# Kernel tuning notes

Hardware: AMD Instinct MI355X
Metric: run time of the kernel (lower is better)

## Reference

```python
import jax, jax.numpy as jnp
import numpy as np
import math
from jax import lax

B, C, L = 8, 512, 1024
NCONV, K, H = 4, 7, 8
DH = C // H
EPS = 1e-5
NEG = -1e30


def layer_norm(x, g, b):
    mu = jnp.mean(x, axis=-1, keepdims=True)
    var = jnp.mean(jnp.square(x - mu), axis=-1, keepdims=True)
    return (x - mu) * lax.rsqrt(var + EPS) * g + b


def positional_encoding(d, n):
    pos = jnp.arange(n, dtype=jnp.float32)[:, None]                     # [n,1]
    div = jnp.exp(jnp.arange(0, d, 2, dtype=jnp.float32) * (-math.log(10000.0) / d))
    ang = pos * div                                                      # [n,d/2]
    pe = jnp.zeros((d, n), dtype=jnp.float32)
    pe = pe.at[0::2].set(jnp.sin(ang).T).at[1::2].set(jnp.cos(ang).T)
    return pe                                                            # [d,n]


def setup_inputs() -> dict:
    key = jax.random.key(0)
    ks = jax.random.split(key, 20)
    s = 0.02
    inp = {
        "x": jax.random.normal(ks[0], (B, C, L), jnp.float32),
        "mask": jnp.ones((B, L), jnp.float32),
        # conv stack params (stacked over NCONV layers)
        "dw_w": jax.random.normal(ks[1], (NCONV, C, 1, K), jnp.float32) * s,
        "dw_b": jnp.zeros((NCONV, C), jnp.float32),
        "pw_w": jax.random.normal(ks[2], (NCONV, C, C), jnp.float32) * s,
        "pw_b": jnp.zeros((NCONV, C), jnp.float32),
        "ln_conv_g": jnp.ones((NCONV, C), jnp.float32),
        "ln_conv_b": jnp.zeros((NCONV, C), jnp.float32),
        # attention params (torch Linear layout: [out,in])
        "Wq": jax.random.normal(ks[3], (C, C), jnp.float32) * s,
        "bq": jnp.zeros((C,), jnp.float32),
        "Wk": jax.random.normal(ks[4], (C, C), jnp.float32) * s,
        "bk": jnp.zeros((C,), jnp.float32),
        "Wv": jax.random.normal(ks[5], (C, C), jnp.float32) * s,
        "bv": jnp.zeros((C,), jnp.float32),
        "Wo": jax.random.normal(ks[6], (C, C), jnp.float32) * s,
        "bo": jnp.zeros((C,), jnp.float32),
        "ln_att_g": jnp.ones((C,), jnp.float32),
        "ln_att_b": jnp.zeros((C,), jnp.float32),
        # final fc + its layernorm
        "Wf": jax.random.normal(ks[7], (C, C), jnp.float32) * s,
        "bf": jnp.zeros((C,), jnp.float32),
        "ln_fc_g": jnp.ones((C,), jnp.float32),
        "ln_fc_b": jnp.zeros((C,), jnp.float32),
    }
    return inp


def reference(x, mask, dw_w, dw_b, pw_w, pw_b, ln_conv_g, ln_conv_b,
              Wq, bq, Wk, bk, Wv, bv, Wo, bo, ln_att_g, ln_att_b,
              Wf, bf, ln_fc_g, ln_fc_b):
    # positional encoding on channels-first input, then -> [B,L,C]
    out = x + positional_encoding(C, L)[None]          # [B,C,L]; dropout = eval mode (identity)
    out = out.transpose(0, 2, 1)                       # [B,L,C]
    res = out
    for i in range(NCONV):                             # fixed small layer loop
        h = layer_norm(out, ln_conv_g[i], ln_conv_b[i])
        h = h.transpose(0, 2, 1)                       # [B,C,L]
        h = lax.conv_general_dilated(h, dw_w[i], (1,), [(K // 2, K // 2)],
                                     dimension_numbers=("NCH", "OIH", "NCH"),
                                     feature_group_count=C) + dw_b[i][None, :, None]
        h = jnp.einsum("bcl,oc->bol", h, pw_w[i]) + pw_b[i][None, :, None]
        h = jax.nn.relu(h).transpose(0, 2, 1)          # [B,L,C]
        out = h + res
        res = out
    # masked multi-head self-attention
    a = layer_norm(out, ln_att_g, ln_att_b)
    q = (a @ Wq.T + bq).reshape(B, L, H, DH)
    k = (a @ Wk.T + bk).reshape(B, L, H, DH)
    v = (a @ Wv.T + bv).reshape(B, L, H, DH)
    scale = 1.0 / math.sqrt(DH)
    scores = jnp.einsum("blhd,bmhd->bhlm", q, k) * scale   # [B,H,L,L]
    m = mask[:, None, None, :]                              # mask over keys
    scores = scores * m + (1.0 - m) * NEG
    attn = jax.nn.softmax(scores, axis=-1)
    o = jnp.einsum("bhlm,bmhd->blhd", attn, v).reshape(B, L, C)
    o = o @ Wo.T + bo
    out = o + res
    res = out
    # feed-forward (single Linear + relu) with residual
    f = layer_norm(out, ln_fc_g, ln_fc_b)
    f = jax.nn.relu(f @ Wf.T + bf)
    out = f + res
    return out
```

## Files before the change

kernel.cpp:

```cpp
#include <hip/hip_runtime.h>
#include <hip/hip_bf16.h>

#define L_SEQ 1024
#define CCH   512
#define NB    8

typedef __bf16 bf16_t;
typedef __bf16 bf16x4 __attribute__((ext_vector_type(4)));
typedef __bf16 bf16x8 __attribute__((ext_vector_type(8)));
typedef float  f32x4  __attribute__((ext_vector_type(4)));

__device__ __forceinline__ void gload_lds16(const void* g, void* l) {
  __builtin_amdgcn_global_load_lds((const __attribute__((address_space(1))) void*)g,
                                   (__attribute__((address_space(3))) void*)l, 16, 0, 0);
}

__global__ __launch_bounds__(256) void cvtall_kernel(
    const float* __restrict__ pw_w, const float* __restrict__ Wq,
    const float* __restrict__ Wk, const float* __restrict__ Wv,
    const float* __restrict__ Wo, const float* __restrict__ Wf,
    const float* __restrict__ dw_w,
    bf16_t* __restrict__ WPW, bf16_t* __restrict__ WQKV,
    bf16_t* __restrict__ WOB, bf16_t* __restrict__ WFB,
    float* __restrict__ WT, float* __restrict__ PET) {
  int idx = blockIdx.x * 256 + threadIdx.x;
  if (idx < 1048576) { WPW[idx] = (bf16_t)pw_w[idx]; return; }
  idx -= 1048576;
  if (idx < 262144) { WQKV[idx] = (bf16_t)Wq[idx]; return; }
  idx -= 262144;
  if (idx < 262144) { WQKV[262144 + idx] = (bf16_t)Wk[idx]; return; }
  idx -= 262144;
  if (idx < 262144) { WQKV[524288 + idx] = (bf16_t)Wv[idx]; return; }
  idx -= 262144;
  if (idx < 262144) { WOB[idx] = (bf16_t)Wo[idx]; return; }
  idx -= 262144;
  if (idx < 262144) { WFB[idx] = (bf16_t)Wf[idx]; return; }
  idx -= 262144;
  if (idx < 14336) {
    int i = idx / 3584, r = idx % 3584, t = r >> 9, c = r & 511;
    WT[idx] = dw_w[i * 3584 + c * 7 + t];
    return;
  }
  idx -= 14336;
  if (idx < 524288) {
    int l = idx >> 9, c = idx & 511;
    float div = expf(-(float)(2 * (c >> 1)) * (9.210340371976184f / 512.0f));
    float ang = (float)l * div;
    PET[idx] = (c & 1) ? cosf(ang) : sinf(ang);
  }
}

__global__ __launch_bounds__(256) void pe_kernel(const float* __restrict__ x,
                                                 const float* __restrict__ PET,
                                                 float* __restrict__ out) {
  __shared__ float tile[32][33];
  int l0 = blockIdx.x * 32, c0 = blockIdx.y * 32, b = blockIdx.z;
  int tx = threadIdx.x, ty = threadIdx.y;
#pragma unroll
  for (int r = 0; r < 32; r += 8)
    tile[ty + r][tx] = x[(size_t)(b * CCH + c0 + ty + r) * L_SEQ + l0 + tx];
  __syncthreads();
#pragma unroll
  for (int r = 0; r < 32; r += 8) {
    int l = l0 + ty + r, c = c0 + tx;
    out[(size_t)(b * L_SEQ + l) * CCH + c] = tile[tx][ty + r] + PET[l * CCH + c];
  }
}

__global__ __launch_bounds__(256) void stats_kernel(const float* __restrict__ in,
                                                    float* __restrict__ Psum,
                                                    float* __restrict__ Psq) {
  int w = threadIdx.x >> 6, l = threadIdx.x & 63;
  int row = blockIdx.x * 4 + w;
  const float* p = in + (size_t)row * CCH + l * 8;
  float v[8];
  *(float4*)(&v[0]) = *(const float4*)p;
  *(float4*)(&v[4]) = *(const float4*)(p + 4);
  float s = 0.f, q = 0.f;
#pragma unroll
  for (int j = 0; j < 8; j++) { s += v[j]; q += v[j] * v[j]; }
  s += __shfl_xor(s, 1); q += __shfl_xor(q, 1);
  s += __shfl_xor(s, 2); q += __shfl_xor(q, 2);
  s += __shfl_xor(s, 4); q += __shfl_xor(q, 4);
  if ((l & 7) == 0) {
    Psum[row * 8 + (l >> 3)] = s;
    Psq[row * 8 + (l >> 3)] = q;
  }
}

__global__ __launch_bounds__(256) void ln_apply_kernel(const float* __restrict__ in,
                                                       const float* __restrict__ Psum,
                                                       const float* __restrict__ Psq,
                                                       const float* __restrict__ gam,
                                                       const float* __restrict__ bet,
                                                       bf16_t* __restrict__ out) {
  int w = threadIdx.x >> 6, l = threadIdx.x & 63;
  int row = blockIdx.x * 4 + w;
  float v0 = 0.f;
  if (l < 8) v0 = Psum[row * 8 + l];
  else if (l < 16) v0 = Psq[row * 8 + (l - 8)];
  v0 += __shfl_xor(v0, 1); v0 += __shfl_xor(v0, 2); v0 += __shfl_xor(v0, 4);
  float sum = __shfl(v0, 0), sq = __shfl(v0, 8);
  float mean = sum * (1.0f / 512.0f);
  float var = sq * (1.0f / 512.0f) - mean * mean;
  float inv = rsqrtf(var + 1e-5f);
  const float* p = in + (size_t)row * CCH + l * 8;
  float v[8], gv[8], bv[8];
  *(float4*)(&v[0]) = *(const float4*)p;
  *(float4*)(&v[4]) = *(const float4*)(p + 4);
  *(float4*)(&gv[0]) = *(const float4*)(gam + l * 8);
  *(float4*)(&gv[4]) = *(const float4*)(gam + l * 8 + 4);
  *(float4*)(&bv[0]) = *(const float4*)(bet + l * 8);
  *(float4*)(&bv[4]) = *(const float4*)(bet + l * 8 + 4);
  bf16x8 o;
#pragma unroll
  for (int j = 0; j < 8; j++) o[j] = (bf16_t)((v[j] - mean) * inv * gv[j] + bv[j]);
  *(bf16x8*)(out + (size_t)row * CCH + l * 8) = o;
}

__global__ __launch_bounds__(256) void dwln_kernel(const float* __restrict__ in,
                                                   const float* __restrict__ Psum,
                                                   const float* __restrict__ Psq,
                                                   const float* __restrict__ gam,
                                                   const float* __restrict__ bet,
                                                   const float* __restrict__ wtt,
                                                   const float* __restrict__ dbias,
                                                   bf16_t* __restrict__ out) {
  int idx = blockIdx.x * 256 + threadIdx.x;
  int lane = threadIdx.x & 63;
  int row = idx >> 6;
  int l = row & (L_SEQ - 1);
  float m_ = 0.f, i_ = 0.f;
  if (lane < 7) {
    int ll = l + lane - 3;
    if (ll >= 0 && ll < L_SEQ) {
      int rr = row + lane - 3;
      float s = 0.f, q = 0.f;
#pragma unroll
      for (int c = 0; c < 8; c++) { s += Psum[rr * 8 + c]; q += Psq[rr * 8 + c]; }
      float mm = s * (1.0f / 512.0f);
      m_ = mm;
      i_ = rsqrtf(q * (1.0f / 512.0f) - mm * mm + 1e-5f);
    }
  }
  float gv[8], bv[8], acc[8];
  *(float4*)&gv[0] = *(const float4*)(gam + lane * 8);
  *(float4*)&gv[4] = *(const float4*)(gam + lane * 8 + 4);
  *(float4*)&bv[0] = *(const float4*)(bet + lane * 8);
  *(float4*)&bv[4] = *(const float4*)(bet + lane * 8 + 4);
  *(float4*)&acc[0] = *(const float4*)(dbias + lane * 8);
  *(float4*)&acc[4] = *(const float4*)(dbias + lane * 8 + 4);
#pragma unroll
  for (int t = 0; t < 7; t++) {
    float mt = __shfl(m_, t), it = __shfl(i_, t);
    int ll = l + t - 3;
    if (ll >= 0 && ll < L_SEQ) {
      const float* p = in + (size_t)(row + t - 3) * CCH + lane * 8;
      float v[8], wv[8];
      *(float4*)&v[0] = *(const float4*)p;
      *(float4*)&v[4] = *(const float4*)(p + 4);
      *(float4*)&wv[0] = *(const float4*)(wtt + t * CCH + lane * 8);
      *(float4*)&wv[4] = *(const float4*)(wtt + t * CCH + lane * 8 + 4);
#pragma unroll
      for (int j = 0; j < 8; j++)
        acc[j] += ((v[j] - mt) * it * gv[j] + bv[j]) * wv[j];
    }
  }
  bf16x8 o;
#pragma unroll
  for (int j = 0; j < 8; j++) o[j] = (bf16_t)acc[j];
  *(bf16x8*)&out[(size_t)row * CCH + lane * 8] = o;
}

#define GEMM_STAGE(SRCA, SRCB, BI, K0)                                            \
  do {                                                                            \
    {                                                                             \
      int row_ = w * 8 + srow;                                                    \
      int off_ = (scb ^ ((row_ & 7) << 4)) >> 1;                                  \
      gload_lds16(SRCA + (size_t)(m0 + row_) * CCH + (K0) + off_,                 \
                  &As[BI][(w * 8) * 64]);                                         \
    }                                                                             \
    _Pragma("unroll") for (int cc = 0; cc < 8; cc++) {                            \
      int row_ = cc * 32 + w * 8 + srow;                                          \
      int off_ = (scb ^ ((row_ & 7) << 4)) >> 1;                                  \
      gload_lds16(SRCB + (size_t)(n0 + row_) * CCH + (K0) + off_,                 \
                  &Bs[BI][(cc * 32 + w * 8) * 64]);                               \
    }                                                                             \
  } while (0)

#define GEMM_COMPUTE(BI)                                                          \
  do {                                                                            \
    _Pragma("unroll") for (int ks = 0; ks < 2; ks++) {                            \
      bf16x8 fa[2], fb[4];                                                        \
      _Pragma("unroll") for (int i = 0; i < 2; i++) {                             \
        int ra = i * 16 + lc;                                                     \
        fa[i] = *(const bf16x8*)&As[BI][ra * 64 +                                 \
                 (((ks * 64 + lg * 16) ^ ((ra & 7) << 4)) >> 1)];                 \
      }                                                                           \
      _Pragma("unroll") for (int j = 0; j < 4; j++) {                             \
        int rb = w * 64 + j * 16 + lc;                                            \
        fb[j] = *(const bf16x8*)&Bs[BI][rb * 64 +                                 \
                 (((ks * 64 + lg * 16) ^ ((rb & 7) << 4)) >> 1)];                 \
      }                                                                           \
      _Pragma("unroll") for (int i = 0; i < 2; i++)                               \
        _Pragma("unroll") for (int j = 0; j < 4; j++)                             \
          acc[i][j] = __builtin_amdgcn_mfma_f32_16x16x32_bf16(fa[i], fb[j],       \
                                                              acc[i][j], 0, 0, 0);\
    }                                                                             \
  } while (0)

template <int RELU, int RES, int BF16OUT, int STATS>
__global__ __launch_bounds__(256) void gemm_kernel(const bf16_t* __restrict__ A,
                                                   const bf16_t* __restrict__ W,
                                                   const float* __restrict__ bias,
                                                   const float* __restrict__ res,
                                                   float* __restrict__ outf,
                                                   bf16_t* __restrict__ outb,
                                                   float* __restrict__ Psum,
                                                   float* __restrict__ Psq) {
  __shared__ __align__(16) bf16_t As[2][32 * 64];
  __shared__ __align__(16) bf16_t Bs[2][256 * 64];
  int tid = threadIdx.x;
  int w = tid >> 6, l = tid & 63;
  int m0 = blockIdx.x * 32, n0 = blockIdx.y * 256;
  int lc = l & 15, lg = l >> 4;
  int srow = l >> 3, scb = (l & 7) * 16;
  f32x4 acc[2][4];
#pragma unroll
  for (int i = 0; i < 2; i++)
#pragma unroll
    for (int j = 0; j < 4; j++) acc[i][j] = f32x4{0.f, 0.f, 0.f, 0.f};

  GEMM_STAGE(A, W, 0, 0);
  __syncthreads();
  int cur = 0;
  for (int t = 0; t < 8; t++) {
    if (t < 7) GEMM_STAGE(A, W, cur ^ 1, (t + 1) * 64);
    GEMM_COMPUTE(cur);
    __syncthreads();
    cur ^= 1;
  }

  float ps[2][4], pq[2][4];
  if (STATS) {
#pragma unroll
    for (int i = 0; i < 2; i++)
#pragma unroll
      for (int r = 0; r < 4; r++) { ps[i][r] = 0.f; pq[i][r] = 0.f; }
  }
#pragma unroll
  for (int i = 0; i < 2; i++) {
    int mbase = m0 + i * 16 + lg * 4;
#pragma unroll
    for (int j = 0; j < 4; j++) {
      int n = n0 + w * 64 + j * 16 + lc;
      float bn = bias[n];
#pragma unroll
      for (int r = 0; r < 4; r++) {
        int m = mbase + r;
        float v2 = acc[i][j][r] + bn;
        if (RELU) v2 = fmaxf(v2, 0.f);
        if (RES) v2 += res[(size_t)m * CCH + n];
        if (BF16OUT) outb[(size_t)m * CCH + n] = (bf16_t)v2;
        else outf[(size_t)m * CCH + n] = v2;
        if (STATS) { ps[i][r] += v2; pq[i][r] += v2 * v2; }
      }
    }
  }
  if (STATS) {
    int chunk = blockIdx.y * 4 + w;
#pragma unroll
    for (int i = 0; i < 2; i++)
#pragma unroll
      for (int r = 0; r < 4; r++) {
        float s = ps[i][r], q = pq[i][r];
        s += __shfl_xor(s, 1); q += __shfl_xor(q, 1);
        s += __shfl_xor(s, 2); q += __shfl_xor(q, 2);
        s += __shfl_xor(s, 4); q += __shfl_xor(q, 4);
        s += __shfl_xor(s, 8); q += __shfl_xor(q, 8);
        if (lc == 0) {
          int row = m0 + i * 16 + lg * 4 + r;
          Psum[row * 8 + chunk] = s;
          Psq[row * 8 + chunk] = q;
        }
      }
  }
}

__global__ __launch_bounds__(256) void qkv_kernel(const bf16_t* __restrict__ A,
                                                  const bf16_t* __restrict__ Wqkv,
                                                  const float* __restrict__ bq,
                                                  const float* __restrict__ bk,
                                                  const float* __restrict__ bv,
                                                  bf16_t* __restrict__ QB,
                                                  bf16_t* __restrict__ KB,
                                                  bf16_t* __restrict__ VT) {
  __shared__ __align__(16) bf16_t As[2][32 * 64];
  __shared__ __align__(16) bf16_t Bs[2][256 * 64];
  int tid = threadIdx.x;
  int w = tid >> 6, l = tid & 63;
  int m0 = blockIdx.x * 32, n0 = blockIdx.y * 256;
  int sec = n0 >> 9;
  int lc = l & 15, lg = l >> 4;
  int srow = l >> 3, scb = (l & 7) * 16;
  f32x4 acc[2][4];
#pragma unroll
  for (int i = 0; i < 2; i++)
#pragma unroll
    for (int j = 0; j < 4; j++) acc[i][j] = f32x4{0.f, 0.f, 0.f, 0.f};

  GEMM_STAGE(A, Wqkv, 0, 0);
  __syncthreads();
  int cur = 0;
  for (int t = 0; t < 8; t++) {
    if (t < 7) GEMM_STAGE(A, Wqkv, cur ^ 1, (t + 1) * 64);
    GEMM_COMPUTE(cur);
    __syncthreads();
    cur ^= 1;
  }

  const float* bp = (sec == 0) ? bq : (sec == 1) ? bk : bv;
#pragma unroll
  for (int i = 0; i < 2; i++) {
    int mbase = m0 + i * 16 + lg * 4;
#pragma unroll
    for (int j = 0; j < 4; j++) {
      int n = n0 + w * 64 + j * 16 + lc;
      int nl = n & 511;
      float bn = bp[nl];
      if (sec < 2) {
        bf16_t* ob = (sec == 0) ? QB : KB;
#pragma unroll
        for (int r = 0; r < 4; r++)
          ob[(size_t)(mbase + r) * CCH + nl] = (bf16_t)(acc[i][j][r] + bn);
      } else {
        int h = nl >> 6, d = nl & 63;
        int b = mbase >> 10, lpos = mbase & 1023;
        bf16x4 t;
#pragma unroll
        for (int r = 0; r < 4; r++) t[r] = (bf16_t)(acc[i][j][r] + bn);
        *(bf16x4*)&VT[(((size_t)(b * 8 + h) * 64 + d) * L_SEQ) + lpos] = t;
      }
    }
  }
}

#define ATT_STAGE(BI, KC)                                                         \
  do {                                                                            \
    _Pragma("unroll") for (int r = 0; r < 2; r++) {                               \
      int row = r * 32 + w * 8 + srow;                                            \
      int sc = (scb ^ ((row & 7) << 4)) >> 1;                                     \
      int key = (KC) * 64 + row;                                                  \
      gload_lds16(K + ((size_t)(b * L_SEQ + key) * CCH + h * 64 + sc),            \
                  &Ks[BI][(r * 32 + w * 8) * 64]);                                \
      gload_lds16(VT + (((size_t)(b * 8 + h) * 64 + row) * L_SEQ + (KC) * 64 + sc),\
                  &Vs[BI][(r * 32 + w * 8) * 64]);                                \
    }                                                                             \
  } while (0)

__global__ __launch_bounds__(256) void attn_kernel(const bf16_t* __restrict__ Q,
                                                   const bf16_t* __restrict__ K,
                                                   const bf16_t* __restrict__ VT,
                                                   const float* __restrict__ mask,
                                                   bf16_t* __restrict__ O) {
  __shared__ __align__(16) bf16_t Ks[2][64 * 64];
  __shared__ __align__(16) bf16_t Vs[2][64 * 64];
  __shared__ __align__(16) bf16_t Pl[4][16 * 64];
  int tid = threadIdx.x;
  int w = tid >> 6, l = tid & 63;
  int bid = blockIdx.x;
  int sw = (bid & 7) * 64 + (bid >> 3);
  int qb = sw & 7, h = (sw >> 3) & 7, b = sw >> 6;
  int lg = l >> 4, lc = l & 15;

  bf16x8 qf[2][2];
#pragma unroll
  for (int s = 0; s < 2; s++) {
    int qrow = qb * 128 + s * 64 + w * 16 + lc;
    const bf16_t* qptr = Q + ((size_t)(b * L_SEQ + qrow) * CCH + h * 64);
    qf[s][0] = *(const bf16x8*)(qptr + lg * 8);
    qf[s][1] = *(const bf16x8*)(qptr + 32 + lg * 8);
  }

  f32x4 oacc[2][4];
  float psl[2][4];
#pragma unroll
  for (int s = 0; s < 2; s++)
#pragma unroll
    for (int nf = 0; nf < 4; nf++) {
      oacc[s][nf] = f32x4{0.f, 0.f, 0.f, 0.f};
      psl[s][nf] = 0.f;
    }

  int srow = l >> 3;
  int scb = (l & 7) * 16;

  ATT_STAGE(0, 0);
  __syncthreads();
  int cur = 0;
  for (int kc = 0; kc < 16; kc++) {
    if (kc < 15) ATT_STAGE(cur ^ 1, kc + 1);

    float mv[4];
#pragma unroll
    for (int kf = 0; kf < 4; kf++) mv[kf] = mask[b * L_SEQ + kc * 64 + kf * 16 + lc];

#pragma unroll
    for (int s = 0; s < 2; s++) {
      f32x4 sacc[4];
#pragma unroll
      for (int kf = 0; kf < 4; kf++) sacc[kf] = f32x4{0.f, 0.f, 0.f, 0.f};
      __builtin_amdgcn_s_setprio(1);
#pragma unroll
      for (int kf = 0; kf < 4; kf++) {
        int row = kf * 16 + lc;
        int sx = (row & 7) << 4;
        const bf16_t* kr = &Ks[cur][row * 64];
        bf16x8 b0 = *(const bf16x8*)(kr + (((lg * 16) ^ sx) >> 1));
        sacc[kf] = __builtin_amdgcn_mfma_f32_16x16x32_bf16(qf[s][0], b0, sacc[kf], 0, 0, 0);
        bf16x8 b1 = *(const bf16x8*)(kr + (((64 + lg * 16) ^ sx) >> 1));
        sacc[kf] = __builtin_amdgcn_mfma_f32_16x16x32_bf16(qf[s][1], b1, sacc[kf], 0, 0, 0);
      }
      __builtin_amdgcn_s_setprio(0);

#pragma unroll
      for (int kf = 0; kf < 4; kf++) {
        float mneg = (1.f - mv[kf]) * (-1e30f);
        float msc = 0.125f * mv[kf];
#pragma unroll
        for (int j = 0; j < 4; j++) {
          float p = __expf(sacc[kf][j] * msc + mneg);
          psl[s][j] += p;
          int q = lg * 4 + j;
          int cb = (kf * 32 + lc * 2) ^ ((q & 7) << 4);
          Pl[w][(q * 128 + cb) >> 1] = (bf16_t)p;
        }
      }

      int sp = (lc & 7) << 4;
      bf16x8 pa0 = *(const bf16x8*)&Pl[w][(lc * 128 + ((lg * 16) ^ sp)) >> 1];
      bf16x8 pa1 = *(const bf16x8*)&Pl[w][(lc * 128 + ((64 + lg * 16) ^ sp)) >> 1];
      __builtin_amdgcn_s_setprio(1);
#pragma unroll
      for (int nf = 0; nf < 4; nf++) {
        int d = nf * 16 + lc;
        int sx = (d & 7) << 4;
        const bf16_t* vr = &Vs[cur][d * 64];
        bf16x8 vb0 = *(const bf16x8*)(vr + (((lg * 16) ^ sx) >> 1));
        oacc[s][nf] = __builtin_amdgcn_mfma_f32_16x16x32_bf16(pa0, vb0, oacc[s][nf], 0, 0, 0);
        bf16x8 vb1 = *(const bf16x8*)(vr + (((64 + lg * 16) ^ sx) >> 1));
        oacc[s][nf] = __builtin_amdgcn_mfma_f32_16x16x32_bf16(pa1, vb1, oacc[s][nf], 0, 0, 0);
      }
      __builtin_amdgcn_s_setprio(0);
    }
    __syncthreads();
    cur ^= 1;
  }

#pragma unroll
  for (int off = 1; off < 16; off <<= 1)
#pragma unroll
    for (int s = 0; s < 2; s++)
#pragma unroll
      for (int j = 0; j < 4; j++) psl[s][j] += __shfl_xor(psl[s][j], off);

#pragma unroll
  for (int s = 0; s < 2; s++)
#pragma unroll
    for (int j = 0; j < 4; j++) {
      float is = 1.0f / psl[s][j];
      int r = qb * 128 + s * 64 + w * 16 + lg * 4 + j;
      bf16_t* op = O + ((size_t)(b * L_SEQ + r) * CCH + h * 64);
#pragma unroll
      for (int nf = 0; nf < 4; nf++) op[nf * 16 + lc] = (bf16_t)(oacc[s][nf][j] * is);
    }
}

extern "C" void kernel_launch(void* const* d_in, const int* in_sizes, int n_in,
                              void* d_out, int out_size, void* d_ws, size_t ws_size,
                              hipStream_t stream) {
  const float* x = (const float*)d_in[0];
  const float* mask = (const float*)d_in[1];
  const float* dw_w = (const float*)d_in[2];
  const float* dw_b = (const float*)d_in[3];
  const float* pw_w = (const float*)d_in[4];
  const float* pw_b = (const float*)d_in[5];
  const float* ln_conv_g = (const float*)d_in[6];
  const float* ln_conv_b = (const float*)d_in[7];
  const float* Wq = (const float*)d_in[8];  const float* bq = (const float*)d_in[9];
  const float* Wk = (const float*)d_in[10]; const float* bk = (const float*)d_in[11];
  const float* Wv = (const float*)d_in[12]; const float* bv = (const float*)d_in[13];
  const float* Wo = (const float*)d_in[14]; const float* bo = (const float*)d_in[15];
  const float* ln_att_g = (const float*)d_in[16]; const float* ln_att_b = (const float*)d_in[17];
  const float* Wf = (const float*)d_in[18]; const float* bfc = (const float*)d_in[19];
  const float* ln_fc_g = (const float*)d_in[20]; const float* ln_fc_b = (const float*)d_in[21];

  float* OUT = (float*)d_out;

  char* ws = (char*)d_ws;
  bf16_t* ABF  = (bf16_t*)(ws);
  bf16_t* QB   = (bf16_t*)(ws + (8u << 20));
  bf16_t* KB   = (bf16_t*)(ws + (16u << 20));
  bf16_t* VT   = (bf16_t*)(ws + (24u << 20));
  char*   wb   = ws + (32u << 20);
  bf16_t* WPW  = (bf16_t*)(wb);
  bf16_t* WQKV = (bf16_t*)(wb + (2u << 20));
  bf16_t* WOB  = (bf16_t*)(wb + 3584u * 1024);
  bf16_t* WFB  = (bf16_t*)(wb + (4u << 20));
  float*  WT   = (float*)(wb + 4608u * 1024);
  float*  PET  = (float*)(ws + (37u << 20));
  float*  Psum = (float*)(ws + (39u << 20));
  float*  Psq  = (float*)(ws + (39u << 20) + 262144);

  cvtall_kernel<<<11320, 256, 0, stream>>>(pw_w, Wq, Wk, Wv, Wo, Wf, dw_w,
                                           WPW, WQKV, WOB, WFB, WT, PET);
  pe_kernel<<<dim3(32, 16, NB), dim3(32, 8), 0, stream>>>(x, PET, OUT);
  stats_kernel<<<2048, 256, 0, stream>>>(OUT, Psum, Psq);

  dim3 ggrid(256, 2);
  for (int i = 0; i < 4; i++) {
    dwln_kernel<<<2048, 256, 0, stream>>>(OUT, Psum, Psq, ln_conv_g + i * 512,
                                          ln_conv_b + i * 512, WT + i * 3584,
                                          dw_b + i * 512, ABF);
    gemm_kernel<1, 1, 0, 1><<<ggrid, 256, 0, stream>>>(ABF, WPW + i * 262144,
                                                       pw_b + i * 512, OUT, OUT,
                                                       nullptr, Psum, Psq);
  }
  ln_apply_kernel<<<2048, 256, 0, stream>>>(OUT, Psum, Psq, ln_att_g, ln_att_b, ABF);
  qkv_kernel<<<dim3(256, 6), 256, 0, stream>>>(ABF, WQKV, bq, bk, bv, QB, KB, VT);
  attn_kernel<<<512, 256, 0, stream>>>(QB, KB, VT, mask, ABF);
  gemm_kernel<0, 1, 0, 1><<<ggrid, 256, 0, stream>>>(ABF, WOB, bo, OUT, OUT,
                                                     nullptr, Psum, Psq);
  ln_apply_kernel<<<2048, 256, 0, stream>>>(OUT, Psum, Psq, ln_fc_g, ln_fc_b, ABF);
  gemm_kernel<1, 1, 0, 0><<<ggrid, 256, 0, stream>>>(ABF, WFB, bfc, OUT,
                                                     (float*)d_out, nullptr,
                                                     nullptr, nullptr);
}
```

Measured before the change: 359.2 us.

## Fuse PE/transpose/stats into prep kernel and retile residual GEMM to 64x128

Merges the weight conversion, positional-encoding add with transpose, and row-statistics kernels into one launch that computes PE inline and emits 16 partial sums per row. The residual GEMM is retiled from 32x256 to 64x128 blocks with a 2x2 wave layout, and Psum/Psq are widened to 16 chunks per row. s_setprio is added around the MFMA sections. This cuts two launches and the PET table round trip, and gives the GEMMs a more balanced tile, at the cost of recomputing sin/cos per element and more partial-stat reads in the LN consumers.

```diff
diff --git a/kernel.cpp b/kernel.cpp
--- a/kernel.cpp
+++ b/kernel.cpp
@@ -15,15 +15,49 @@
                                    (__attribute__((address_space(3))) void*)l, 16, 0, 0);
 }
 
-__global__ __launch_bounds__(256) void cvtall_kernel(
+__global__ __launch_bounds__(256) void prep_kernel(
+    const float* __restrict__ x, const float* __restrict__ PET_in,
     const float* __restrict__ pw_w, const float* __restrict__ Wq,
     const float* __restrict__ Wk, const float* __restrict__ Wv,
     const float* __restrict__ Wo, const float* __restrict__ Wf,
     const float* __restrict__ dw_w,
     bf16_t* __restrict__ WPW, bf16_t* __restrict__ WQKV,
     bf16_t* __restrict__ WOB, bf16_t* __restrict__ WFB,
-    float* __restrict__ WT, float* __restrict__ PET) {
-  int idx = blockIdx.x * 256 + threadIdx.x;
+    float* __restrict__ WT, float* __restrict__ PET,
+    float* __restrict__ out, float* __restrict__ Psum, float* __restrict__ Psq) {
+  int blk = blockIdx.x;
+  if (blk < 4096) {
+    __shared__ float tile[32][33];
+    int bx = blk & 31, by = (blk >> 5) & 15, b = blk >> 9;
+    int l0 = bx * 32, c0 = by * 32;
+    int tx = threadIdx.x & 31, ty = threadIdx.x >> 5;
+#pragma unroll
+    for (int r = 0; r < 32; r += 8)
+      tile[ty + r][tx] = x[(size_t)(b * CCH + c0 + ty + r) * L_SEQ + l0 + tx];
+    __syncthreads();
+#pragma unroll
+    for (int r = 0; r < 32; r += 8) {
+      int l = l0 + ty + r, c = c0 + tx;
+      float div = expf(-(float)(2 * (c >> 1)) * (9.210340371976184f / 512.0f));
+      float ang = (float)l * div;
+      float pe = (c & 1) ? cosf(ang) : sinf(ang);
+      float v = tile[tx][ty + r] + pe;
+      out[(size_t)(b * L_SEQ + l) * CCH + c] = v;
+      float s = v, q = v * v;
+#pragma unroll
+      for (int off = 1; off < 32; off <<= 1) {
+        s += __shfl_xor(s, off);
+        q += __shfl_xor(q, off);
+      }
+      if (tx == 0) {
+        size_t row = (size_t)(b * L_SEQ + l);
+        Psum[row * 16 + (c0 >> 5)] = s;
+        Psq[row * 16 + (c0 >> 5)] = q;
+      }
+    }
+    return;
+  }
+  int idx = (blk - 4096) * 256 + threadIdx.x;
   if (idx < 1048576) { WPW[idx] = (bf16_t)pw_w[idx]; return; }
   idx -= 1048576;
   if (idx < 262144) { WQKV[idx] = (bf16_t)Wq[idx]; return; }
@@ -39,53 +73,8 @@
   if (idx < 14336) {
     int i = idx / 3584, r = idx % 3584, t = r >> 9, c = r & 511;
     WT[idx] = dw_w[i * 3584 + c * 7 + t];
-    return;
-  }
-  idx -= 14336;
-  if (idx < 524288) {
-    int l = idx >> 9, c = idx & 511;
-    float div = expf(-(float)(2 * (c >> 1)) * (9.210340371976184f / 512.0f));
-    float ang = (float)l * div;
-    PET[idx] = (c & 1) ? cosf(ang) : sinf(ang);
-  }
-}
-
-__global__ __launch_bounds__(256) void pe_kernel(const float* __restrict__ x,
-                                                 const float* __restrict__ PET,
-                                                 float* __restrict__ out) {
-  __shared__ float tile[32][33];
-  int l0 = blockIdx.x * 32, c0 = blockIdx.y * 32, b = blockIdx.z;
-  int tx = threadIdx.x, ty = threadIdx.y;
-#pragma unroll
-  for (int r = 0; r < 32; r += 8)
-    tile[ty + r][tx] = x[(size_t)(b * CCH + c0 + ty + r) * L_SEQ + l0 + tx];
-  __syncthreads();
-#pragma unroll
-  for (int r = 0; r < 32; r += 8) {
-    int l = l0 + ty + r, c = c0 + tx;
-    out[(size_t)(b * L_SEQ + l) * CCH + c] = tile[tx][ty + r] + PET[l * CCH + c];
-  }
-}
-
-__global__ __launch_bounds__(256) void stats_kernel(const float* __restrict__ in,
-                                                    float* __restrict__ Psum,
-                                                    float* __restrict__ Psq) {
-  int w = threadIdx.x >> 6, l = threadIdx.x & 63;
-  int row = blockIdx.x * 4 + w;
-  const float* p = in + (size_t)row * CCH + l * 8;
-  float v[8];
-  *(float4*)(&v[0]) = *(const float4*)p;
-  *(float4*)(&v[4]) = *(const float4*)(p + 4);
-  float s = 0.f, q = 0.f;
-#pragma unroll
-  for (int j = 0; j < 8; j++) { s += v[j]; q += v[j] * v[j]; }
-  s += __shfl_xor(s, 1); q += __shfl_xor(q, 1);
-  s += __shfl_xor(s, 2); q += __shfl_xor(q, 2);
-  s += __shfl_xor(s, 4); q += __shfl_xor(q, 4);
-  if ((l & 7) == 0) {
-    Psum[row * 8 + (l >> 3)] = s;
-    Psq[row * 8 + (l >> 3)] = q;
-  }
+  }
+  (void)PET_in; (void)PET;
 }
 
 __global__ __launch_bounds__(256) void ln_apply_kernel(const float* __restrict__ in,
@@ -97,10 +86,11 @@
   int w = threadIdx.x >> 6, l = threadIdx.x & 63;
   int row = blockIdx.x * 4 + w;
   float v0 = 0.f;
-  if (l < 8) v0 = Psum[row * 8 + l];
-  else if (l < 16) v0 = Psq[row * 8 + (l - 8)];
-  v0 += __shfl_xor(v0, 1); v0 += __shfl_xor(v0, 2); v0 += __shfl_xor(v0, 4);
-  float sum = __shfl(v0, 0), sq = __shfl(v0, 8);
+  if (l < 16) v0 = Psum[(size_t)row * 16 + l];
+  else if (l < 32) v0 = Psq[(size_t)row * 16 + (l - 16)];
+  v0 += __shfl_xor(v0, 1); v0 += __shfl_xor(v0, 2);
+  v0 += __shfl_xor(v0, 4); v0 += __shfl_xor(v0, 8);
+  float sum = __shfl(v0, 0), sq = __shfl(v0, 16);
   float mean = sum * (1.0f / 512.0f);
   float var = sq * (1.0f / 512.0f) - mean * mean;
   float inv = rsqrtf(var + 1e-5f);
@@ -137,7 +127,7 @@
       int rr = row + lane - 3;
       float s = 0.f, q = 0.f;
 #pragma unroll
-      for (int c = 0; c < 8; c++) { s += Psum[rr * 8 + c]; q += Psq[rr * 8 + c]; }
+      for (int c = 0; c < 16; c++) { s += Psum[(size_t)rr * 16 + c]; q += Psq[(size_t)rr * 16 + c]; }
       float mm = s * (1.0f / 512.0f);
       m_ = mm;
       i_ = rsqrtf(q * (1.0f / 512.0f) - mm * mm + 1e-5f);
@@ -172,6 +162,123 @@
   *(bf16x8*)&out[(size_t)row * CCH + lane * 8] = o;
 }
 
+#define GSTAGE64(SRCA, SRCB, BI, K0)                                              \
+  do {                                                                            \
+    _Pragma("unroll") for (int cc = 0; cc < 2; cc++) {                            \
+      int row_ = cc * 32 + w * 8 + srow;                                          \
+      int off_ = (scb ^ ((row_ & 7) << 4)) >> 1;                                  \
+      gload_lds16(SRCA + (size_t)(m0 + row_) * CCH + (K0) + off_,                 \
+                  &As[BI][(cc * 32 + w * 8) * 64]);                               \
+    }                                                                             \
+    _Pragma("unroll") for (int cc = 0; cc < 4; cc++) {                            \
+      int row_ = cc * 32 + w * 8 + srow;                                          \
+      int off_ = (scb ^ ((row_ & 7) << 4)) >> 1;                                  \
+      gload_lds16(SRCB + (size_t)(n0 + row_) * CCH + (K0) + off_,                 \
+                  &Bs[BI][(cc * 32 + w * 8) * 64]);                               \
+    }                                                                             \
+  } while (0)
+
+#define GCOMP64(BI)                                                               \
+  do {                                                                            \
+    __builtin_amdgcn_s_setprio(1);                                                \
+    _Pragma("unroll") for (int ks = 0; ks < 2; ks++) {                            \
+      bf16x8 fa[2], fb[4];                                                        \
+      _Pragma("unroll") for (int i = 0; i < 2; i++) {                             \
+        int ra = wr * 32 + i * 16 + lc;                                           \
+        fa[i] = *(const bf16x8*)&As[BI][ra * 64 +                                 \
+                 (((ks * 64 + lg * 16) ^ ((ra & 7) << 4)) >> 1)];                 \
+      }                                                                           \
+      _Pragma("unroll") for (int j = 0; j < 4; j++) {                             \
+        int rb = wc * 64 + j * 16 + lc;                                           \
+        fb[j] = *(const bf16x8*)&Bs[BI][rb * 64 +                                 \
+                 (((ks * 64 + lg * 16) ^ ((rb & 7) << 4)) >> 1)];                 \
+      }                                                                           \
+      _Pragma("unroll") for (int i = 0; i < 2; i++)                               \
+        _Pragma("unroll") for (int j = 0; j < 4; j++)                             \
+          acc[i][j] = __builtin_amdgcn_mfma_f32_16x16x32_bf16(fa[i], fb[j],       \
+                                                              acc[i][j], 0, 0, 0);\
+    }                                                                             \
+    __builtin_amdgcn_s_setprio(0);                                                \
+  } while (0)
+
+template <int RELU, int RES, int BF16OUT, int STATS>
+__global__ __launch_bounds__(256) void gemm_kernel(const bf16_t* __restrict__ A,
+                                                   const bf16_t* __restrict__ W,
+                                                   const float* __restrict__ bias,
+                                                   const float* __restrict__ res,
+                                                   float* __restrict__ outf,
+                                                   bf16_t* __restrict__ outb,
+                                                   float* __restrict__ Psum,
+                                                   float* __restrict__ Psq) {
+  __shared__ __align__(16) bf16_t As[2][64 * 64];
+  __shared__ __align__(16) bf16_t Bs[2][128 * 64];
+  int tid = threadIdx.x;
+  int w = tid >> 6, l = tid & 63;
+  int m0 = blockIdx.x * 64, n0 = blockIdx.y * 128;
+  int wr = w >> 1, wc = w & 1;
+  int lc = l & 15, lg = l >> 4;
+  int srow = l >> 3, scb = (l & 7) * 16;
+  f32x4 acc[2][4];
+#pragma unroll
+  for (int i = 0; i < 2; i++)
+#pragma unroll
+    for (int j = 0; j < 4; j++) acc[i][j] = f32x4{0.f, 0.f, 0.f, 0.f};
+
+  GSTAGE64(A, W, 0, 0);
+  __syncthreads();
+  int cur = 0;
+  for (int t = 0; t < 8; t++) {
+    if (t < 7) GSTAGE64(A, W, cur ^ 1, (t + 1) * 64);
+    GCOMP64(cur);
+    __syncthreads();
+    cur ^= 1;
+  }
+
+#pragma unroll
+  for (int i = 0; i < 2; i++) {
+    int mbase = m0 + wr * 32 + i * 16 + lg * 4;
+    float ps[2][4], pq[2][4];
+    if (STATS) {
+#pragma unroll
+      for (int jh = 0; jh < 2; jh++)
+#pragma unroll
+        for (int r = 0; r < 4; r++) { ps[jh][r] = 0.f; pq[jh][r] = 0.f; }
+    }
+#pragma unroll
+    for (int j = 0; j < 4; j++) {
+      int n = n0 + wc * 64 + j * 16 + lc;
+      float bn = bias[n];
+#pragma unroll
+      for (int r = 0; r < 4; r++) {
+        int m = mbase + r;
+        float v2 = acc[i][j][r] + bn;
+        if (RELU) v2 = fmaxf(v2, 0.f);
+        if (RES) v2 += res[(size_t)m * CCH + n];
+        if (BF16OUT) outb[(size_t)m * CCH + n] = (bf16_t)v2;
+        else outf[(size_t)m * CCH + n] = v2;
+        if (STATS) { ps[j >> 1][r] += v2; pq[j >> 1][r] += v2 * v2; }
+      }
+    }
+    if (STATS) {
+#pragma unroll
+      for (int jh = 0; jh < 2; jh++)
+#pragma unroll
+        for (int r = 0; r < 4; r++) {
+          float s = ps[jh][r], q = pq[jh][r];
+          s += __shfl_xor(s, 1); q += __shfl_xor(q, 1);
+          s += __shfl_xor(s, 2); q += __shfl_xor(q, 2);
+          s += __shfl_xor(s, 4); q += __shfl_xor(q, 4);
+          s += __shfl_xor(s, 8); q += __shfl_xor(q, 8);
+          if (lc == 0) {
+            size_t row = mbase + r;
+            Psum[row * 16 + blockIdx.y * 4 + wc * 2 + jh] = s;
+            Psq[row * 16 + blockIdx.y * 4 + wc * 2 + jh] = q;
+          }
+        }
+    }
+  }
+}
+
 #define GEMM_STAGE(SRCA, SRCB, BI, K0)                                            \
   do {                                                                            \
     {                                                                             \
@@ -190,6 +297,7 @@
 
 #define GEMM_COMPUTE(BI)                                                          \
   do {                                                                            \
+    __builtin_amdgcn_s_setprio(1);                                                \
     _Pragma("unroll") for (int ks = 0; ks < 2; ks++) {                            \
       bf16x8 fa[2], fb[4];                                                        \
       _Pragma("unroll") for (int i = 0; i < 2; i++) {                             \
@@ -207,85 +315,8 @@
           acc[i][j] = __builtin_amdgcn_mfma_f32_16x16x32_bf16(fa[i], fb[j],       \
                                                               acc[i][j], 0, 0, 0);\
     }                                                                             \
+    __builtin_amdgcn_s_setprio(0);                                                \
   } while (0)
-
-template <int RELU, int RES, int BF16OUT, int STATS>
-__global__ __launch_bounds__(256) void gemm_kernel(const bf16_t* __restrict__ A,
-                                                   const bf16_t* __restrict__ W,
-                                                   const float* __restrict__ bias,
-                                                   const float* __restrict__ res,
-                                                   float* __restrict__ outf,
-                                                   bf16_t* __restrict__ outb,
-                                                   float* __restrict__ Psum,
-                                                   float* __restrict__ Psq) {
-  __shared__ __align__(16) bf16_t As[2][32 * 64];
-  __shared__ __align__(16) bf16_t Bs[2][256 * 64];
-  int tid = threadIdx.x;
-  int w = tid >> 6, l = tid & 63;
-  int m0 = blockIdx.x * 32, n0 = blockIdx.y * 256;
-  int lc = l & 15, lg = l >> 4;
-  int srow = l >> 3, scb = (l & 7) * 16;
-  f32x4 acc[2][4];
-#pragma unroll
-  for (int i = 0; i < 2; i++)
-#pragma unroll
-    for (int j = 0; j < 4; j++) acc[i][j] = f32x4{0.f, 0.f, 0.f, 0.f};
-
-  GEMM_STAGE(A, W, 0, 0);
-  __syncthreads();
-  int cur = 0;
-  for (int t = 0; t < 8; t++) {
-    if (t < 7) GEMM_STAGE(A, W, cur ^ 1, (t + 1) * 64);
-    GEMM_COMPUTE(cur);
-    __syncthreads();
-    cur ^= 1;
-  }
-
-  float ps[2][4], pq[2][4];
-  if (STATS) {
-#pragma unroll
-    for (int i = 0; i < 2; i++)
-#pragma unroll
-      for (int r = 0; r < 4; r++) { ps[i][r] = 0.f; pq[i][r] = 0.f; }
-  }
-#pragma unroll
-  for (int i = 0; i < 2; i++) {
-    int mbase = m0 + i * 16 + lg * 4;
-#pragma unroll
-    for (int j = 0; j < 4; j++) {
-      int n = n0 + w * 64 + j * 16 + lc;
-      float bn = bias[n];
-#pragma unroll
-      for (int r = 0; r < 4; r++) {
-        int m = mbase + r;
-        float v2 = acc[i][j][r] + bn;
-        if (RELU) v2 = fmaxf(v2, 0.f);
-        if (RES) v2 += res[(size_t)m * CCH + n];
-        if (BF16OUT) outb[(size_t)m * CCH + n] = (bf16_t)v2;
-        else outf[(size_t)m * CCH + n] = v2;
-        if (STATS) { ps[i][r] += v2; pq[i][r] += v2 * v2; }
-      }
-    }
-  }
-  if (STATS) {
-    int chunk = blockIdx.y * 4 + w;
-#pragma unroll
-    for (int i = 0; i < 2; i++)
-#pragma unroll
-      for (int r = 0; r < 4; r++) {
-        float s = ps[i][r], q = pq[i][r];
-        s += __shfl_xor(s, 1); q += __shfl_xor(q, 1);
-        s += __shfl_xor(s, 2); q += __shfl_xor(q, 2);
-        s += __shfl_xor(s, 4); q += __shfl_xor(q, 4);
-        s += __shfl_xor(s, 8); q += __shfl_xor(q, 8);
-        if (lc == 0) {
-          int row = m0 + i * 16 + lg * 4 + r;
-          Psum[row * 8 + chunk] = s;
-          Psq[row * 8 + chunk] = q;
-        }
-      }
-  }
-}
 
 __global__ __launch_bounds__(256) void qkv_kernel(const bf16_t* __restrict__ A,
                                                   const bf16_t* __restrict__ Wqkv,
@@ -510,14 +541,13 @@
   float*  WT   = (float*)(wb + 4608u * 1024);
   float*  PET  = (float*)(ws + (37u << 20));
   float*  Psum = (float*)(ws + (39u << 20));
-  float*  Psq  = (float*)(ws + (39u << 20) + 262144);
-
-  cvtall_kernel<<<11320, 256, 0, stream>>>(pw_w, Wq, Wk, Wv, Wo, Wf, dw_w,
-                                           WPW, WQKV, WOB, WFB, WT, PET);
-  pe_kernel<<<dim3(32, 16, NB), dim3(32, 8), 0, stream>>>(x, PET, OUT);
-  stats_kernel<<<2048, 256, 0, stream>>>(OUT, Psum, Psq);
-
-  dim3 ggrid(256, 2);
+  float*  Psq  = (float*)(ws + (39u << 20) + 524288);
+
+  prep_kernel<<<15416, 256, 0, stream>>>(x, PET, pw_w, Wq, Wk, Wv, Wo, Wf, dw_w,
+                                         WPW, WQKV, WOB, WFB, WT, PET,
+                                         OUT, Psum, Psq);
+
+  dim3 ggrid(128, 4);
   for (int i = 0; i < 4; i++) {
     dwln_kernel<<<2048, 256, 0, stream>>>(OUT, Psum, Psq, ln_conv_g + i * 512,
                                           ln_conv_b + i * 512, WT + i * 3584,
```

Result: no change. 353.0 us (-1.7%).
